# Kernel tuning notes

Hardware: AMD Instinct MI355X
Metric: run time of the kernel (lower is better)

Reference implementation:

```python
import jax, jax.numpy as jnp
import numpy as np

B, N, D = 4, 4096, 1024

def setup_inputs() -> dict:
    key = jax.random.key(0)
    kx, kql, kqr, kk, kv = jax.random.split(key, 5)
    std = 1.0 / D
    return {
        "x": jax.random.normal(kx, (B, N, D), dtype=jnp.float32),
        "w_query_left": jax.random.normal(kql, (D, D), dtype=jnp.float32) * std,
        "w_query_right": jax.random.normal(kqr, (D, D), dtype=jnp.float32) * std,
        "w_key": jax.random.normal(kk, (D, D), dtype=jnp.float32) * std,
        "w_value": jax.random.normal(kv, (D, D), dtype=jnp.float32) * std,
    }

def reference(x, w_query_left, w_query_right, w_key, w_value):
    # Four dxd projections
    query_left = jnp.einsum('bnd,de->bne', x, w_query_left)
    query_right = jnp.einsum('bnd,de->bne', x, w_query_right)
    key = jnp.einsum('bnd,de->bne', x, w_key)
    value = jnp.einsum('bnd,de->bne', x, w_value)
    # Elementwise gate
    query = query_left * query_right
    # Kernelized attention: key^T @ value, then query @ kv  (dropout p=0 in eval)
    kv_attn = jnp.einsum('bnd,bne->bde', key, value)   # [B, D, D]
    linear_attn = jnp.einsum('bnd,bde->bne', query, kv_attn)
    return linear_attn
```

## Files before the change

kernel.cpp:

```cpp
#include <hip/hip_runtime.h>
#include <stdint.h>

typedef short bf16x8 __attribute__((ext_vector_type(8)));
typedef float f32x4 __attribute__((ext_vector_type(4)));

__device__ __forceinline__ uint16_t f2b(float f) {
    uint32_t u = __builtin_bit_cast(uint32_t, f);
    return (uint16_t)((u + 0x7fffu + ((u >> 16) & 1u)) >> 16);
}

__device__ __forceinline__ void gll16(const void* g, void* l) {
    __builtin_amdgcn_global_load_lds(
        (const __attribute__((address_space(1))) uint32_t*)(uintptr_t)g,
        (__attribute__((address_space(3))) uint32_t*)(uint32_t)(uintptr_t)l,
        16, 0, 0);
}

__global__ __launch_bounds__(256) void cvt_tr(const float* __restrict__ x,
                                              uint16_t* __restrict__ xb,
                                              uint16_t* __restrict__ xT) {
    const int b = blockIdx.z;
    const int n0 = blockIdx.y * 64;
    const int d0 = blockIdx.x * 64;
    __shared__ uint16_t tile[64][66];
    const int t = threadIdx.x;
    const float* xbase = x + (size_t)b * 4194304;
#pragma unroll
    for (int p = 0; p < 4; p++) {
        int row = p * 16 + (t >> 4);
        int c4 = (t & 15) * 4;
        float4 v = *(const float4*)&xbase[(size_t)(n0 + row) * 1024 + d0 + c4];
        uint16_t b0 = f2b(v.x), b1 = f2b(v.y), b2 = f2b(v.z), b3 = f2b(v.w);
        tile[row][c4 + 0] = b0;
        tile[row][c4 + 1] = b1;
        tile[row][c4 + 2] = b2;
        tile[row][c4 + 3] = b3;
        uint2 pk;
        pk.x = (uint32_t)b0 | ((uint32_t)b1 << 16);
        pk.y = (uint32_t)b2 | ((uint32_t)b3 << 16);
        *(uint2*)&xb[(size_t)(b * 4096 + n0 + row) * 1024 + d0 + c4] = pk;
    }
    __syncthreads();
    uint16_t* oT = xT + (size_t)b * 4194304;
#pragma unroll
    for (int p = 0; p < 4; p++) {
        int a = p * 16 + (t >> 4);
        int b4 = (t & 15) * 4;
        uint32_t x0 = tile[b4 + 0][a], x1 = tile[b4 + 1][a];
        uint32_t x2 = tile[b4 + 2][a], x3 = tile[b4 + 3][a];
        uint2 pk;
        pk.x = x0 | (x1 << 16);
        pk.y = x2 | (x3 << 16);
        *(uint2*)&oT[(size_t)(d0 + a) * 4096 + n0 + b4] = pk;
    }
}

struct Ptr4 { const float* p[4]; };

__global__ __launch_bounds__(256) void tr_w(Ptr4 wp, uint16_t* __restrict__ out) {
    const int m = blockIdx.z;
    const float* in = wp.p[m];
    uint16_t* o = out + (size_t)m * 1048576;
    __shared__ uint16_t tile[64][68];
    int t = threadIdx.x;
    int r0 = blockIdx.y * 64, c0 = blockIdx.x * 64;
    for (int p = 0; p < 4; p++) {
        int row = p * 16 + (t >> 4);
        int c4 = (t & 15) * 4;
        float4 v = *(const float4*)&in[(size_t)(r0 + row) * 1024 + c0 + c4];
        tile[row][c4 + 0] = f2b(v.x);
        tile[row][c4 + 1] = f2b(v.y);
        tile[row][c4 + 2] = f2b(v.z);
        tile[row][c4 + 3] = f2b(v.w);
    }
    __syncthreads();
    for (int p = 0; p < 4; p++) {
        int a = p * 16 + (t >> 4);
        int b4 = (t & 15) * 4;
        uint32_t x0 = tile[b4 + 0][a], x1 = tile[b4 + 1][a];
        uint32_t x2 = tile[b4 + 2][a], x3 = tile[b4 + 3][a];
        uint2 pk;
        pk.x = x0 | (x1 << 16);
        pk.y = x2 | (x3 << 16);
        *(uint2*)&o[(size_t)(c0 + a) * 1024 + r0 + b4] = pk;
    }
}

__global__ __launch_bounds__(512, 2) void proj_gate8(const uint16_t* __restrict__ A,
                                                     const uint16_t* __restrict__ Wt,
                                                     uint16_t* __restrict__ Q) {
    __shared__ uint16_t lds[65536];
    const int t = threadIdx.x;
    const int wave = t >> 6;
    const int lane = t & 63;
    const int m0 = blockIdx.y * 256;
    const int e0 = blockIdx.x * 128;
    const uint16_t* B1 = Wt + (size_t)e0 * 1024;
    const uint16_t* B2 = Wt + 1048576 + (size_t)e0 * 1024;
    const int wm = (wave >> 1) * 64;
    const int wn = (wave & 1) * 64;

    int LsA0 = t * 16;
    int LsA1 = 8192 + t * 16;
    int LsB  = t * 16;
    int gbA0 = LsA0 ^ (((LsA0 >> 7) & 7) << 4);
    int gbA1 = LsA1 ^ (((LsA1 >> 7) & 7) << 4);
    int gbB  = LsB  ^ (((LsB  >> 7) & 7) << 4);
    const uint16_t* srcA0 = A + (size_t)(m0 + (gbA0 >> 6)) * 1024 + ((gbA0 & 63) >> 1);
    const uint16_t* srcA1 = A + (size_t)(m0 + (gbA1 >> 6)) * 1024 + ((gbA1 & 63) >> 1);
    const uint16_t* srcB1 = B1 + (size_t)(gbB >> 6) * 1024 + ((gbB & 63) >> 1);
    const uint16_t* srcB2 = B2 + (size_t)(gbB >> 6) * 1024 + ((gbB & 63) >> 1);

    auto STAGE = [&](int kt_, int ks_) {
        const int h = (2 * kt_ + ks_) & 3;
        const int kb = kt_ * 64 + ks_ * 32;
        uint16_t* db = lds + h * 16384 + (wave << 9);
        gll16(srcA0 + kb, db);
        gll16(srcA1 + kb, db + 4096);
        gll16(srcB1 + kb, db + 8192);
        gll16(srcB2 + kb, db + 12288);
    };

    const int cb = (lane >> 4) << 4;
    int aoff[4], b1off[4], b2off[4];
#pragma unroll
    for (int i = 0; i < 4; i++) {
        int g = (wm + i * 16 + (lane & 15)) * 64 + cb;
        aoff[i] = (g ^ (((g >> 7) & 7) << 4)) >> 1;
    }
#pragma unroll
    for (int j = 0; j < 4; j++) {
        int g = (wn + j * 16 + (lane & 15)) * 64 + cb;
        int sw = (g ^ (((g >> 7) & 7) << 4)) >> 1;
        b1off[j] = 8192 + sw;
        b2off[j] = 12288 + sw;
    }

    f32x4 acc1[4][4] = {};
    f32x4 acc2[4][4] = {};

    STAGE(0, 0); STAGE(0, 1); STAGE(1, 0); STAGE(1, 1);
    asm volatile("s_waitcnt vmcnt(12)" ::: "memory");
    __builtin_amdgcn_s_barrier();

    for (int kt = 0; kt < 16; ++kt) {
        const uint16_t* lb0 = lds + ((2 * kt) & 3) * 16384;
        const uint16_t* lb1 = lds + ((2 * kt + 1) & 3) * 16384;
        bf16x8 af[4], bq[4];

#pragma unroll
        for (int i = 0; i < 4; i++) af[i] = *(const bf16x8*)&lb0[aoff[i]];
#pragma unroll
        for (int j = 0; j < 4; j++) bq[j] = *(const bf16x8*)&lb0[b1off[j]];
        __builtin_amdgcn_s_barrier();
        asm volatile("s_waitcnt lgkmcnt(0)" ::: "memory");
        __builtin_amdgcn_sched_barrier(0);
        __builtin_amdgcn_s_setprio(1);
#pragma unroll
        for (int i = 0; i < 4; i++)
#pragma unroll
            for (int j = 0; j < 4; j++)
                acc1[i][j] = __builtin_amdgcn_mfma_f32_16x16x32_bf16(af[i], bq[j],
                                                                     acc1[i][j], 0, 0, 0);
        __builtin_amdgcn_s_setprio(0);
        __builtin_amdgcn_s_barrier();

#pragma unroll
        for (int j = 0; j < 4; j++) bq[j] = *(const bf16x8*)&lb0[b2off[j]];
        __builtin_amdgcn_s_barrier();
        asm volatile("s_waitcnt lgkmcnt(0)" ::: "memory");
        __builtin_amdgcn_sched_barrier(0);
        __builtin_amdgcn_s_setprio(1);
#pragma unroll
        for (int i = 0; i < 4; i++)
#pragma unroll
            for (int j = 0; j < 4; j++)
                acc2[i][j] = __builtin_amdgcn_mfma_f32_16x16x32_bf16(af[i], bq[j],
                                                                     acc2[i][j], 0, 0, 0);
        __builtin_amdgcn_s_setprio(0);
        if (kt < 15) { asm volatile("s_waitcnt vmcnt(8)" ::: "memory"); }
        else         { asm volatile("s_waitcnt vmcnt(0)" ::: "memory"); }
        __builtin_amdgcn_s_barrier();
        if (kt < 14) STAGE(kt + 2, 0);

#pragma unroll
        for (int i = 0; i < 4; i++) af[i] = *(const bf16x8*)&lb1[aoff[i]];
#pragma unroll
        for (int j = 0; j < 4; j++) bq[j] = *(const bf16x8*)&lb1[b1off[j]];
        __builtin_amdgcn_s_barrier();
        asm volatile("s_waitcnt lgkmcnt(0)" ::: "memory");
        __builtin_amdgcn_sched_barrier(0);
        __builtin_amdgcn_s_setprio(1);
#pragma unroll
        for (int i = 0; i < 4; i++)
#pragma unroll
            for (int j = 0; j < 4; j++)
                acc1[i][j] = __builtin_amdgcn_mfma_f32_16x16x32_bf16(af[i], bq[j],
                                                                     acc1[i][j], 0, 0, 0);
        __builtin_amdgcn_s_setprio(0);
        __builtin_amdgcn_s_barrier();

#pragma unroll
        for (int j = 0; j < 4; j++) bq[j] = *(const bf16x8*)&lb1[b2off[j]];
        __builtin_amdgcn_s_barrier();
        asm volatile("s_waitcnt lgkmcnt(0)" ::: "memory");
        __builtin_amdgcn_sched_barrier(0);
        __builtin_amdgcn_s_setprio(1);
#pragma unroll
        for (int i = 0; i < 4; i++)
#pragma unroll
            for (int j = 0; j < 4; j++)
                acc2[i][j] = __builtin_amdgcn_mfma_f32_16x16x32_bf16(af[i], bq[j],
                                                                     acc2[i][j], 0, 0, 0);
        __builtin_amdgcn_s_setprio(0);
        if (kt < 14)       { asm volatile("s_waitcnt vmcnt(8)" ::: "memory"); }
        else if (kt == 14) { asm volatile("s_waitcnt vmcnt(4)" ::: "memory"); }
        else               { asm volatile("s_waitcnt vmcnt(0)" ::: "memory"); }
        __builtin_amdgcn_s_barrier();
        if (kt < 14) STAGE(kt + 2, 1);
    }

    const int rl = (lane >> 4) * 4;
    const int cl = lane & 15;
#pragma unroll
    for (int i = 0; i < 4; i++)
#pragma unroll
        for (int j = 0; j < 4; j++)
#pragma unroll
            for (int r = 0; r < 4; r++) {
                float g = acc1[i][j][r] * acc2[i][j][r];
                Q[(size_t)(m0 + wm + i * 16 + rl + r) * 1024 + e0 + wn + j * 16 + cl] = f2b(g);
            }
}

__global__ __launch_bounds__(256) void gemm_kv_splitk(const uint16_t* __restrict__ VT,
                                                      const uint16_t* __restrict__ KT,
                                                      float* __restrict__ P) {
    const int z = blockIdx.z;
    const int batch = z >> 1, ks = z & 1;
    const uint16_t* Ab = VT + (size_t)batch * 4194304 + ks * 2048;
    const uint16_t* Bb = KT + (size_t)batch * 4194304 + ks * 2048;

    __shared__ uint16_t lA[4096];
    __shared__ uint16_t lB[4096];

    const int t = threadIdx.x;
    const int wave = t >> 6;
    const int lane = t & 63;
    const int m0 = blockIdx.y * 128;
    const int n0 = blockIdx.x * 128;
    const int wm = (wave >> 1) * 64;
    const int wn = (wave & 1) * 64;

    const uint16_t* gA0 = Ab + (size_t)(m0 + (t >> 2)) * 4096 + (t & 3) * 8;
    const uint16_t* gB0 = Bb + (size_t)(n0 + (t >> 2)) * 4096 + (t & 3) * 8;
    uint16_t* lA0 = lA + wave * 512;
    uint16_t* lA1 = lA + 2048 + wave * 512;
    uint16_t* lB0 = lB + wave * 512;
    uint16_t* lB1 = lB + 2048 + wave * 512;

    f32x4 acc[4][4] = {};

    const int arow = wm + (lane & 15);
    const int brow = wn + (lane & 15);
    const int koff = (lane >> 4) * 8;

    for (int k0 = 0; k0 < 2048; k0 += 32) {
        __syncthreads();
        gll16(gA0 + k0, lA0);
        gll16(gA0 + (size_t)64 * 4096 + k0, lA1);
        gll16(gB0 + k0, lB0);
        gll16(gB0 + (size_t)64 * 4096 + k0, lB1);
        __syncthreads();

        bf16x8 af[4], bfr[4];
#pragma unroll
        for (int i = 0; i < 4; i++)
            af[i] = *(const bf16x8*)&lA[(arow + i * 16) * 32 + koff];
#pragma unroll
        for (int i = 0; i < 4; i++)
            bfr[i] = *(const bf16x8*)&lB[(brow + i * 16) * 32 + koff];
#pragma unroll
        for (int i = 0; i < 4; i++)
#pragma unroll
            for (int j = 0; j < 4; j++)
                acc[i][j] = __builtin_amdgcn_mfma_f32_16x16x32_bf16(af[i], bfr[j],
                                                                    acc[i][j], 0, 0, 0);
    }

    float* Pb = P + (size_t)z * 1048576;
    const int crow = m0 + wm + (lane >> 4) * 4;
    const int ccol = n0 + wn + (lane & 15);
#pragma unroll
    for (int i = 0; i < 4; i++)
#pragma unroll
        for (int j = 0; j < 4; j++)
#pragma unroll
            for (int r = 0; r < 4; r++)
                Pb[(size_t)(crow + i * 16 + r) * 1024 + ccol + j * 16] = acc[i][j][r];
}

__global__ __launch_bounds__(256) void reduce_kv(const float4* __restrict__ P,
                                                 uint2* __restrict__ G) {
    int i = blockIdx.x * 256 + threadIdx.x;
    int b = i >> 18;
    int r = i & 262143;
    const float4* base = P + (size_t)b * 524288 + r;
    float4 s0 = base[0];
    float4 s1 = base[262144];
    float x = s0.x + s1.x;
    float y = s0.y + s1.y;
    float zz = s0.z + s1.z;
    float w = s0.w + s1.w;
    uint2 o;
    o.x = (uint32_t)f2b(x) | ((uint32_t)f2b(y) << 16);
    o.y = (uint32_t)f2b(zz) | ((uint32_t)f2b(w) << 16);
    G[i] = o;
}

__global__ __launch_bounds__(256) void gemm_nt_bf16(const uint16_t* __restrict__ A,
                                                    int lda, int az,
                                                    const uint16_t* __restrict__ Bt,
                                                    int ldb,
                                                    uint16_t* __restrict__ C,
                                                    int ldc, int cz) {
    const uint16_t* Ab = A + (size_t)blockIdx.z * az;
    uint16_t* Cb = C + (size_t)blockIdx.z * cz;

    __shared__ uint16_t lA[4096];
    __shared__ uint16_t lB[4096];

    const int t = threadIdx.x;
    const int wave = t >> 6;
    const int lane = t & 63;
    const int m0 = blockIdx.y * 128;
    const int n0 = blockIdx.x * 128;
    const int wm = (wave >> 1) * 64;
    const int wn = (wave & 1) * 64;

    const uint16_t* gA0 = Ab + (size_t)(m0 + (t >> 2)) * lda + (t & 3) * 8;
    const uint16_t* gB0 = Bt + (size_t)(n0 + (t >> 2)) * ldb + (t & 3) * 8;
    uint16_t* lA0 = lA + wave * 512;
    uint16_t* lA1 = lA + 2048 + wave * 512;
    uint16_t* lB0 = lB + wave * 512;
    uint16_t* lB1 = lB + 2048 + wave * 512;

    f32x4 acc[4][4] = {};

    const int arow = wm + (lane & 15);
    const int brow = wn + (lane & 15);
    const int koff = (lane >> 4) * 8;

    for (int k0 = 0; k0 < 1024; k0 += 32) {
        __syncthreads();
        gll16(gA0 + k0, lA0);
        gll16(gA0 + (size_t)64 * lda + k0, lA1);
        gll16(gB0 + k0, lB0);
        gll16(gB0 + (size_t)64 * ldb + k0, lB1);
        __syncthreads();

        bf16x8 af[4], bfr[4];
#pragma unroll
        for (int i = 0; i < 4; i++)
            af[i] = *(const bf16x8*)&lA[(arow + i * 16) * 32 + koff];
#pragma unroll
        for (int i = 0; i < 4; i++)
            bfr[i] = *(const bf16x8*)&lB[(brow + i * 16) * 32 + koff];
#pragma unroll
        for (int i = 0; i < 4; i++)
#pragma unroll
            for (int j = 0; j < 4; j++)
                acc[i][j] = __builtin_amdgcn_mfma_f32_16x16x32_bf16(af[i], bfr[j],
                                                                    acc[i][j], 0, 0, 0);
    }

    const int crow = m0 + wm + (lane >> 4) * 4;
    const int ccol = n0 + wn + (lane & 15);
#pragma unroll
    for (int i = 0; i < 4; i++)
#pragma unroll
        for (int j = 0; j < 4; j++)
#pragma unroll
            for (int r = 0; r < 4; r++)
                Cb[(size_t)(crow + i * 16 + r) * ldc + ccol + j * 16] = f2b(acc[i][j][r]);
}

__global__ __launch_bounds__(256) void gemm_out(const uint16_t* __restrict__ A,
                                                const uint16_t* __restrict__ Bt,
                                                float* __restrict__ C) {
    const uint16_t* Ab = A + (size_t)blockIdx.z * 4194304;
    const uint16_t* Bb = Bt + (size_t)blockIdx.z * 1048576;

    __shared__ uint16_t lA[4096];
    __shared__ uint16_t lB[4096];

    const int t = threadIdx.x;
    const int wave = t >> 6;
    const int lane = t & 63;
    const int m0 = blockIdx.y * 128;
    const int n0 = blockIdx.x * 128;
    const int wm = (wave >> 1) * 64;
    const int wn = (wave & 1) * 64;

    const uint16_t* gA0 = Ab + (size_t)(m0 + (t >> 2)) * 1024 + (t & 3) * 8;
    const uint16_t* gB0 = Bb + (size_t)(n0 + (t >> 2)) * 1024 + (t & 3) * 8;
    uint16_t* lA0 = lA + wave * 512;
    uint16_t* lA1 = lA + 2048 + wave * 512;
    uint16_t* lB0 = lB + wave * 512;
    uint16_t* lB1 = lB + 2048 + wave * 512;

    f32x4 acc[4][4] = {};

    const int arow = wm + (lane & 15);
    const int brow = wn + (lane & 15);
    const int koff = (lane >> 4) * 8;

    for (int k0 = 0; k0 < 1024; k0 += 32) {
        __syncthreads();
        gll16(gA0 + k0, lA0);
        gll16(gA0 + (size_t)64 * 1024 + k0, lA1);
        gll16(gB0 + k0, lB0);
        gll16(gB0 + (size_t)64 * 1024 + k0, lB1);
        __syncthreads();

        bf16x8 af[4], bfr[4];
#pragma unroll
        for (int i = 0; i < 4; i++)
            af[i] = *(const bf16x8*)&lA[(arow + i * 16) * 32 + koff];
#pragma unroll
        for (int i = 0; i < 4; i++)
            bfr[i] = *(const bf16x8*)&lB[(brow + i * 16) * 32 + koff];
#pragma unroll
        for (int i = 0; i < 4; i++)
#pragma unroll
            for (int j = 0; j < 4; j++)
                acc[i][j] = __builtin_amdgcn_mfma_f32_16x16x32_bf16(af[i], bfr[j],
                                                                    acc[i][j], 0, 0, 0);
    }

    float* Cb = C + (size_t)blockIdx.z * 4194304;
    const int crow = m0 + wm + (lane >> 4) * 4;
    const int ccol = n0 + wn + (lane & 15);
#pragma unroll
    for (int i = 0; i < 4; i++)
#pragma unroll
        for (int j = 0; j < 4; j++)
#pragma unroll
            for (int r = 0; r < 4; r++)
                Cb[(size_t)(crow + i * 16 + r) * 1024 + ccol + j * 16] = acc[i][j][r];
}

extern "C" void kernel_launch(void* const* d_in, const int* in_sizes, int n_in,
                              void* d_out, int out_size, void* d_ws, size_t ws_size,
                              hipStream_t stream) {
    const float* x = (const float*)d_in[0];

    uint16_t* ws  = (uint16_t*)d_ws;
    uint16_t* xb  = ws;
    uint16_t* xT  = ws + 16777216;
    uint16_t* Wt  = ws + 33554432;
    uint16_t* Q   = ws + 37748736;
    float*    P   = (float*)(ws + 54525952);
    uint16_t* G   = ws + 71303168;
    uint16_t* H   = ws + 75497472;
    uint16_t* kvT = ws + 79691776;

    cvt_tr<<<dim3(16, 64, 4), 256, 0, stream>>>(x, xb, xT);

    Ptr4 wp;
    wp.p[0] = (const float*)d_in[1];
    wp.p[1] = (const float*)d_in[2];
    wp.p[2] = (const float*)d_in[3];
    wp.p[3] = (const float*)d_in[4];
    tr_w<<<dim3(16, 16, 4), 256, 0, stream>>>(wp, Wt);

    proj_gate8<<<dim3(8, 64), 512, 0, stream>>>(xb, Wt, Q);

    gemm_kv_splitk<<<dim3(8, 8, 8), 256, 0, stream>>>(xT, xT, P);

    reduce_kv<<<4096, 256, 0, stream>>>((const float4*)P, (uint2*)G);

    gemm_nt_bf16<<<dim3(32, 8, 1), 256, 0, stream>>>(Wt + 3 * 1048576, 1024, 0,
                                                     G, 1024, H, 4096, 0);

    gemm_nt_bf16<<<dim3(8, 8, 4), 256, 0, stream>>>(H, 4096, 1024,
                                                    Wt + 2 * 1048576, 1024,
                                                    kvT, 1024, 1048576);

    gemm_out<<<dim3(8, 32, 4), 256, 0, stream>>>(Q, kvT, (float*)d_out);
}
```

Measured before the change: 389.8 us.

## Merge prep kernels, swizzle block order, and use pipelined 256x256 output GEMM

Combines the x conversion/transpose and weight transpose kernels into a single launch. Adds an XCD-aware block index swizzle to the projection, kv and NT GEMM kernels so neighbouring tiles share L2. Replaces the simple 128x128 output GEMM with a 512-thread 256x256-tile kernel that uses swizzled LDS, a four-deep global-to-LDS prefetch and wave priority hints, which raises data reuse at the cost of more registers and LDS per block.

```diff
diff --git a/kernel.cpp b/kernel.cpp
--- a/kernel.cpp
+++ b/kernel.cpp
@@ -16,73 +16,87 @@
         16, 0, 0);
 }
 
-__global__ __launch_bounds__(256) void cvt_tr(const float* __restrict__ x,
-                                              uint16_t* __restrict__ xb,
-                                              uint16_t* __restrict__ xT) {
-    const int b = blockIdx.z;
-    const int n0 = blockIdx.y * 64;
-    const int d0 = blockIdx.x * 64;
-    __shared__ uint16_t tile[64][66];
+__device__ __forceinline__ void swz3(int& bx, int& by, int& bz) {
+    const int nx = gridDim.x, ny = gridDim.y, nz = gridDim.z;
+    const int n = nx * ny * nz;
+    int orig = blockIdx.x + nx * (blockIdx.y + ny * blockIdx.z);
+    int l = (orig & 7) * (n >> 3) + (orig >> 3);
+    bx = l % nx; l /= nx;
+    by = l % ny;
+    bz = l / ny;
+}
+
+struct Ptr4 { const float* p[4]; };
+
+__global__ __launch_bounds__(256) void prep(const float* __restrict__ x,
+                                            uint16_t* __restrict__ xb,
+                                            uint16_t* __restrict__ xT,
+                                            Ptr4 wp, uint16_t* __restrict__ Wt) {
+    __shared__ uint16_t tile[64][68];
     const int t = threadIdx.x;
-    const float* xbase = x + (size_t)b * 4194304;
-#pragma unroll
-    for (int p = 0; p < 4; p++) {
-        int row = p * 16 + (t >> 4);
-        int c4 = (t & 15) * 4;
-        float4 v = *(const float4*)&xbase[(size_t)(n0 + row) * 1024 + d0 + c4];
-        uint16_t b0 = f2b(v.x), b1 = f2b(v.y), b2 = f2b(v.z), b3 = f2b(v.w);
-        tile[row][c4 + 0] = b0;
-        tile[row][c4 + 1] = b1;
-        tile[row][c4 + 2] = b2;
-        tile[row][c4 + 3] = b3;
-        uint2 pk;
-        pk.x = (uint32_t)b0 | ((uint32_t)b1 << 16);
-        pk.y = (uint32_t)b2 | ((uint32_t)b3 << 16);
-        *(uint2*)&xb[(size_t)(b * 4096 + n0 + row) * 1024 + d0 + c4] = pk;
-    }
-    __syncthreads();
-    uint16_t* oT = xT + (size_t)b * 4194304;
-#pragma unroll
-    for (int p = 0; p < 4; p++) {
-        int a = p * 16 + (t >> 4);
-        int b4 = (t & 15) * 4;
-        uint32_t x0 = tile[b4 + 0][a], x1 = tile[b4 + 1][a];
-        uint32_t x2 = tile[b4 + 2][a], x3 = tile[b4 + 3][a];
-        uint2 pk;
-        pk.x = x0 | (x1 << 16);
-        pk.y = x2 | (x3 << 16);
-        *(uint2*)&oT[(size_t)(d0 + a) * 4096 + n0 + b4] = pk;
-    }
-}
-
-struct Ptr4 { const float* p[4]; };
-
-__global__ __launch_bounds__(256) void tr_w(Ptr4 wp, uint16_t* __restrict__ out) {
-    const int m = blockIdx.z;
-    const float* in = wp.p[m];
-    uint16_t* o = out + (size_t)m * 1048576;
-    __shared__ uint16_t tile[64][68];
-    int t = threadIdx.x;
-    int r0 = blockIdx.y * 64, c0 = blockIdx.x * 64;
-    for (int p = 0; p < 4; p++) {
-        int row = p * 16 + (t >> 4);
-        int c4 = (t & 15) * 4;
-        float4 v = *(const float4*)&in[(size_t)(r0 + row) * 1024 + c0 + c4];
-        tile[row][c4 + 0] = f2b(v.x);
-        tile[row][c4 + 1] = f2b(v.y);
-        tile[row][c4 + 2] = f2b(v.z);
-        tile[row][c4 + 3] = f2b(v.w);
-    }
-    __syncthreads();
-    for (int p = 0; p < 4; p++) {
-        int a = p * 16 + (t >> 4);
-        int b4 = (t & 15) * 4;
-        uint32_t x0 = tile[b4 + 0][a], x1 = tile[b4 + 1][a];
-        uint32_t x2 = tile[b4 + 2][a], x3 = tile[b4 + 3][a];
-        uint2 pk;
-        pk.x = x0 | (x1 << 16);
-        pk.y = x2 | (x3 << 16);
-        *(uint2*)&o[(size_t)(c0 + a) * 1024 + r0 + b4] = pk;
+    int id = blockIdx.x;
+    if (id < 4096) {
+        const int d0 = (id & 15) * 64;
+        const int n0 = ((id >> 4) & 63) * 64;
+        const int b = id >> 10;
+        const float* xbase = x + (size_t)b * 4194304;
+#pragma unroll
+        for (int p = 0; p < 4; p++) {
+            int row = p * 16 + (t >> 4);
+            int c4 = (t & 15) * 4;
+            float4 v = *(const float4*)&xbase[(size_t)(n0 + row) * 1024 + d0 + c4];
+            uint16_t b0 = f2b(v.x), b1 = f2b(v.y), b2 = f2b(v.z), b3 = f2b(v.w);
+            tile[row][c4 + 0] = b0;
+            tile[row][c4 + 1] = b1;
+            tile[row][c4 + 2] = b2;
+            tile[row][c4 + 3] = b3;
+            uint2 pk;
+            pk.x = (uint32_t)b0 | ((uint32_t)b1 << 16);
+            pk.y = (uint32_t)b2 | ((uint32_t)b3 << 16);
+            *(uint2*)&xb[(size_t)(b * 4096 + n0 + row) * 1024 + d0 + c4] = pk;
+        }
+        __syncthreads();
+        uint16_t* oT = xT + (size_t)b * 4194304;
+#pragma unroll
+        for (int p = 0; p < 4; p++) {
+            int a = p * 16 + (t >> 4);
+            int b4 = (t & 15) * 4;
+            uint32_t x0 = tile[b4 + 0][a], x1 = tile[b4 + 1][a];
+            uint32_t x2 = tile[b4 + 2][a], x3 = tile[b4 + 3][a];
+            uint2 pk;
+            pk.x = x0 | (x1 << 16);
+            pk.y = x2 | (x3 << 16);
+            *(uint2*)&oT[(size_t)(d0 + a) * 4096 + n0 + b4] = pk;
+        }
+    } else {
+        id -= 4096;
+        const int c0 = (id & 15) * 64;
+        const int r0 = ((id >> 4) & 15) * 64;
+        const int m = id >> 8;
+        const float* in = wp.p[m];
+        uint16_t* o = Wt + (size_t)m * 1048576;
+#pragma unroll
+        for (int p = 0; p < 4; p++) {
+            int row = p * 16 + (t >> 4);
+            int c4 = (t & 15) * 4;
+            float4 v = *(const float4*)&in[(size_t)(r0 + row) * 1024 + c0 + c4];
+            tile[row][c4 + 0] = f2b(v.x);
+            tile[row][c4 + 1] = f2b(v.y);
+            tile[row][c4 + 2] = f2b(v.z);
+            tile[row][c4 + 3] = f2b(v.w);
+        }
+        __syncthreads();
+#pragma unroll
+        for (int p = 0; p < 4; p++) {
+            int a = p * 16 + (t >> 4);
+            int b4 = (t & 15) * 4;
+            uint32_t x0 = tile[b4 + 0][a], x1 = tile[b4 + 1][a];
+            uint32_t x2 = tile[b4 + 2][a], x3 = tile[b4 + 3][a];
+            uint2 pk;
+            pk.x = x0 | (x1 << 16);
+            pk.y = x2 | (x3 << 16);
+            *(uint2*)&o[(size_t)(c0 + a) * 1024 + r0 + b4] = pk;
+        }
     }
 }
 
@@ -93,8 +107,10 @@
     const int t = threadIdx.x;
     const int wave = t >> 6;
     const int lane = t & 63;
-    const int m0 = blockIdx.y * 256;
-    const int e0 = blockIdx.x * 128;
+    int bx, by, bz;
+    swz3(bx, by, bz);
+    const int m0 = by * 256;
+    const int e0 = bx * 128;
     const uint16_t* B1 = Wt + (size_t)e0 * 1024;
     const uint16_t* B2 = Wt + 1048576 + (size_t)e0 * 1024;
     const int wm = (wave >> 1) * 64;
@@ -102,10 +118,9 @@
 
     int LsA0 = t * 16;
     int LsA1 = 8192 + t * 16;
-    int LsB  = t * 16;
     int gbA0 = LsA0 ^ (((LsA0 >> 7) & 7) << 4);
     int gbA1 = LsA1 ^ (((LsA1 >> 7) & 7) << 4);
-    int gbB  = LsB  ^ (((LsB  >> 7) & 7) << 4);
+    int gbB  = LsA0 ^ (((LsA0 >> 7) & 7) << 4);
     const uint16_t* srcA0 = A + (size_t)(m0 + (gbA0 >> 6)) * 1024 + ((gbA0 & 63) >> 1);
     const uint16_t* srcA1 = A + (size_t)(m0 + (gbA1 >> 6)) * 1024 + ((gbA1 & 63) >> 1);
     const uint16_t* srcB1 = B1 + (size_t)(gbB >> 6) * 1024 + ((gbB & 63) >> 1);
@@ -233,10 +248,125 @@
             }
 }
 
+__global__ __launch_bounds__(512, 2) void gemm_out8(const uint16_t* __restrict__ A,
+                                                    const uint16_t* __restrict__ kvT,
+                                                    float* __restrict__ C) {
+    __shared__ uint16_t lds[65536];
+    const int t = threadIdx.x;
+    const int wave = t >> 6;
+    const int lane = t & 63;
+    int bx, by, bz;
+    swz3(bx, by, bz);
+    const int m0 = by * 256;
+    const int n0 = bx * 256;
+    const int batch = by >> 4;
+    const uint16_t* Bb = kvT + (size_t)batch * 1048576 + (size_t)n0 * 1024;
+    const int wm = (wave >> 2) * 128;
+    const int wn = (wave & 3) * 64;
+
+    int Ls0 = t * 16;
+    int Ls1 = 8192 + t * 16;
+    int gb0 = Ls0 ^ (((Ls0 >> 7) & 7) << 4);
+    int gb1 = Ls1 ^ (((Ls1 >> 7) & 7) << 4);
+    const uint16_t* srcA0 = A + (size_t)(m0 + (gb0 >> 6)) * 1024 + ((gb0 & 63) >> 1);
+    const uint16_t* srcA1 = A + (size_t)(m0 + (gb1 >> 6)) * 1024 + ((gb1 & 63) >> 1);
+    const uint16_t* srcB0 = Bb + (size_t)(gb0 >> 6) * 1024 + ((gb0 & 63) >> 1);
+    const uint16_t* srcB1 = Bb + (size_t)(gb1 >> 6) * 1024 + ((gb1 & 63) >> 1);
+
+    auto STAGE = [&](int kt_, int ks_) {
+        const int h = (2 * kt_ + ks_) & 3;
+        const int kb = kt_ * 64 + ks_ * 32;
+        uint16_t* db = lds + h * 16384 + (wave << 9);
+        gll16(srcA0 + kb, db);
+        gll16(srcA1 + kb, db + 4096);
+        gll16(srcB0 + kb, db + 8192);
+        gll16(srcB1 + kb, db + 12288);
+    };
+
+    const int cb = (lane >> 4) << 4;
+    int aoff[8], boff[4];
+#pragma unroll
+    for (int i = 0; i < 8; i++) {
+        int g = (wm + i * 16 + (lane & 15)) * 64 + cb;
+        aoff[i] = (g ^ (((g >> 7) & 7) << 4)) >> 1;
+    }
+#pragma unroll
+    for (int j = 0; j < 4; j++) {
+        int g = (wn + j * 16 + (lane & 15)) * 64 + cb;
+        boff[j] = 8192 + ((g ^ (((g >> 7) & 7) << 4)) >> 1);
+    }
+
+    f32x4 acc[8][4] = {};
+
+    STAGE(0, 0); STAGE(0, 1); STAGE(1, 0); STAGE(1, 1);
+    asm volatile("s_waitcnt vmcnt(12)" ::: "memory");
+    __builtin_amdgcn_s_barrier();
+
+    for (int kt = 0; kt < 16; ++kt) {
+        const uint16_t* lb0 = lds + ((2 * kt) & 3) * 16384;
+        const uint16_t* lb1 = lds + ((2 * kt + 1) & 3) * 16384;
+        bf16x8 af[8], bq[4];
+
+#pragma unroll
+        for (int i = 0; i < 8; i++) af[i] = *(const bf16x8*)&lb0[aoff[i]];
+#pragma unroll
+        for (int j = 0; j < 4; j++) bq[j] = *(const bf16x8*)&lb0[boff[j]];
+        __builtin_amdgcn_s_barrier();
+        asm volatile("s_waitcnt lgkmcnt(0)" ::: "memory");
+        __builtin_amdgcn_sched_barrier(0);
+        __builtin_amdgcn_s_setprio(1);
+#pragma unroll
+        for (int i = 0; i < 8; i++)
+#pragma unroll
+            for (int j = 0; j < 4; j++)
+                acc[i][j] = __builtin_amdgcn_mfma_f32_16x16x32_bf16(af[i], bq[j],
+                                                                    acc[i][j], 0, 0, 0);
+        __builtin_amdgcn_s_setprio(0);
+        if (kt < 15) { asm volatile("s_waitcnt vmcnt(8)" ::: "memory"); }
+        else         { asm volatile("s_waitcnt vmcnt(0)" ::: "memory"); }
+        __builtin_amdgcn_s_barrier();
+        if (kt < 14) STAGE(kt + 2, 0);
+
+#pragma unroll
+        for (int i = 0; i < 8; i++) af[i] = *(const bf16x8*)&lb1[aoff[i]];
+#pragma unroll
+        for (int j = 0; j < 4; j++) bq[j] = *(const bf16x8*)&lb1[boff[j]];
+        __builtin_amdgcn_s_barrier();
+        asm volatile("s_waitcnt lgkmcnt(0)" ::: "memory");
+        __builtin_amdgcn_sched_barrier(0);
+        __builtin_amdgcn_s_setprio(1);
+#pragma unroll
+        for (int i = 0; i < 8; i++)
+#pragma unroll
+            for (int j = 0; j < 4; j++)
+                acc[i][j] = __builtin_amdgcn_mfma_f32_16x16x32_bf16(af[i], bq[j],
+                                                                    acc[i][j], 0, 0, 0);
+        __builtin_amdgcn_s_setprio(0);
+        if (kt < 14)       { asm volatile("s_waitcnt vmcnt(8)" ::: "memory"); }
+        else if (kt == 14) { asm volatile("s_waitcnt vmcnt(4)" ::: "memory"); }
+        else               { asm volatile("s_waitcnt vmcnt(0)" ::: "memory"); }
+        __builtin_amdgcn_s_barrier();
+        if (kt < 14) STAGE(kt + 2, 1);
+    }
+
+    const int rl = (lane >> 4) * 4;
+    const int cl = lane & 15;
+#pragma unroll
+    for (int i = 0; i < 8; i++)
+#pragma unroll
+        for (int j = 0; j < 4; j++)
+#pragma unroll
+            for (int r = 0; r < 4; r++)
+                C[(size_t)(m0 + wm + i * 16 + rl + r) * 1024 + n0 + wn + j * 16 + cl] =
+                    acc[i][j][r];
+}
+
 __global__ __launch_bounds__(256) void gemm_kv_splitk(const uint16_t* __restrict__ VT,
                                                       const uint16_t* __restrict__ KT,
                                                       float* __restrict__ P) {
-    const int z = blockIdx.z;
+    int bxs, bys, bzs;
+    swz3(bxs, bys, bzs);
+    const int z = bzs;
     const int batch = z >> 1, ks = z & 1;
     const uint16_t* Ab = VT + (size_t)batch * 4194304 + ks * 2048;
     const uint16_t* Bb = KT + (size_t)batch * 4194304 + ks * 2048;
@@ -247,8 +377,8 @@
     const int t = threadIdx.x;
     const int wave = t >> 6;
     const int lane = t & 63;
-    const int m0 = blockIdx.y * 128;
-    const int n0 = blockIdx.x * 128;
+    const int m0 = bys * 128;
+    const int n0 = bxs * 128;
     const int wm = (wave >> 1) * 64;
     const int wn = (wave & 1) * 64;
 
@@ -324,8 +454,10 @@
                                                     int ldb,
                                                     uint16_t* __restrict__ C,
                                                     int ldc, int cz) {
-    const uint16_t* Ab = A + (size_t)blockIdx.z * az;
-    uint16_t* Cb = C + (size_t)blockIdx.z * cz;
+    int bxs, bys, bzs;
+    swz3(bxs, bys, bzs);
+    const uint16_t* Ab = A + (size_t)bzs * az;
+    uint16_t* Cb = C + (size_t)bzs * cz;
 
     __shared__ uint16_t lA[4096];
     __shared__ uint16_t lB[4096];
@@ -333,8 +465,8 @@
     const int t = threadIdx.x;
     const int wave = t >> 6;
     const int lane = t & 63;
-    const int m0 = blockIdx.y * 128;
-    const int n0 = blockIdx.x * 128;
+    const int m0 = bys * 128;
+    const int n0 = bxs * 128;
     const int wm = (wave >> 1) * 64;
     const int wn = (wave & 1) * 64;
 
@@ -383,71 +515,6 @@
 #pragma unroll
             for (int r = 0; r < 4; r++)
                 Cb[(size_t)(crow + i * 16 + r) * ldc + ccol + j * 16] = f2b(acc[i][j][r]);
-}
-
-__global__ __launch_bounds__(256) void gemm_out(const uint16_t* __restrict__ A,
-                                                const uint16_t* __restrict__ Bt,
-                                                float* __restrict__ C) {
-    const uint16_t* Ab = A + (size_t)blockIdx.z * 4194304;
-    const uint16_t* Bb = Bt + (size_t)blockIdx.z * 1048576;
-
-    __shared__ uint16_t lA[4096];
-    __shared__ uint16_t lB[4096];
-
-    const int t = threadIdx.x;
-    const int wave = t >> 6;
-    const int lane = t & 63;
-    const int m0 = blockIdx.y * 128;
-    const int n0 = blockIdx.x * 128;
-    const int wm = (wave >> 1) * 64;
-    const int wn = (wave & 1) * 64;
-
-    const uint16_t* gA0 = Ab + (size_t)(m0 + (t >> 2)) * 1024 + (t & 3) * 8;
-    const uint16_t* gB0 = Bb + (size_t)(n0 + (t >> 2)) * 1024 + (t & 3) * 8;
-    uint16_t* lA0 = lA + wave * 512;
-    uint16_t* lA1 = lA + 2048 + wave * 512;
-    uint16_t* lB0 = lB + wave * 512;
-    uint16_t* lB1 = lB + 2048 + wave * 512;
-
-    f32x4 acc[4][4] = {};
-
-    const int arow = wm + (lane & 15);
-    const int brow = wn + (lane & 15);
-    const int koff = (lane >> 4) * 8;
-
-    for (int k0 = 0; k0 < 1024; k0 += 32) {
-        __syncthreads();
-        gll16(gA0 + k0, lA0);
-        gll16(gA0 + (size_t)64 * 1024 + k0, lA1);
-        gll16(gB0 + k0, lB0);
-        gll16(gB0 + (size_t)64 * 1024 + k0, lB1);
-        __syncthreads();
-
-        bf16x8 af[4], bfr[4];
-#pragma unroll
-        for (int i = 0; i < 4; i++)
-            af[i] = *(const bf16x8*)&lA[(arow + i * 16) * 32 + koff];
-#pragma unroll
-        for (int i = 0; i < 4; i++)
-            bfr[i] = *(const bf16x8*)&lB[(brow + i * 16) * 32 + koff];
-#pragma unroll
-        for (int i = 0; i < 4; i++)
-#pragma unroll
-            for (int j = 0; j < 4; j++)
-                acc[i][j] = __builtin_amdgcn_mfma_f32_16x16x32_bf16(af[i], bfr[j],
-                                                                    acc[i][j], 0, 0, 0);
-    }
-
-    float* Cb = C + (size_t)blockIdx.z * 4194304;
-    const int crow = m0 + wm + (lane >> 4) * 4;
-    const int ccol = n0 + wn + (lane & 15);
-#pragma unroll
-    for (int i = 0; i < 4; i++)
-#pragma unroll
-        for (int j = 0; j < 4; j++)
-#pragma unroll
-            for (int r = 0; r < 4; r++)
-                Cb[(size_t)(crow + i * 16 + r) * 1024 + ccol + j * 16] = acc[i][j][r];
 }
 
 extern "C" void kernel_launch(void* const* d_in, const int* in_sizes, int n_in,
@@ -465,14 +532,12 @@
     uint16_t* H   = ws + 75497472;
     uint16_t* kvT = ws + 79691776;
 
-    cvt_tr<<<dim3(16, 64, 4), 256, 0, stream>>>(x, xb, xT);
-
     Ptr4 wp;
     wp.p[0] = (const float*)d_in[1];
     wp.p[1] = (const float*)d_in[2];
     wp.p[2] = (const float*)d_in[3];
     wp.p[3] = (const float*)d_in[4];
-    tr_w<<<dim3(16, 16, 4), 256, 0, stream>>>(wp, Wt);
+    prep<<<5120, 256, 0, stream>>>(x, xb, xT, wp, Wt);
 
     proj_gate8<<<dim3(8, 64), 512, 0, stream>>>(xb, Wt, Q);
 
@@ -487,5 +552,5 @@
                                                     Wt + 2 * 1048576, 1024,
                                                     kvT, 1024, 1048576);
 
-    gemm_out<<<dim3(8, 32, 4), 256, 0, stream>>>(Q, kvT, (float*)d_out);
-}
+    gemm_out8<<<dim3(4, 64), 512, 0, stream>>>(Q, kvT, (float*)d_out);
+}
```

Measured after the change: 351.3 us. -9.9%, faster.
